# Kernel tuning notes

Measured on AMD Instinct MI355X. Metric: run time of the kernel, lower is better.

The kernel has to match this reference:

```python
import jax, jax.numpy as jnp
import numpy as np

MULTI_INFER_NUM = 8
D_EMBED = 128
T, B = 512, 32


def setup_inputs() -> dict:
    key = jax.random.key(0)
    k1, k2, k3 = jax.random.split(key, 3)
    positions = jax.random.randint(k1, (T, B), 0, 16, dtype=jnp.int64)
    outputs = jax.random.normal(k2, (T, B, D_EMBED), dtype=jnp.float32)
    table = jax.random.normal(k3, (MULTI_INFER_NUM + 1, D_EMBED, D_EMBED), dtype=jnp.float32)
    return {"positions": positions, "outputs": outputs, "table": table}


def reference(positions, outputs, table):
    # clip positions >= multi_infer_num to the sentinel row multi_infer_num
    r_positions = jnp.where(positions < MULTI_INFER_NUM, positions, MULTI_INFER_NUM)
    # gather per-(t,b) d x d transfer matrices: [T, B, d, d]
    positions_embedding = table[r_positions]
    # batched matvec: [T, B, d]
    transferred = jnp.einsum('ibde,ibd->ibe', positions_embedding, outputs)
    return transferred
```

## Files before the change

kernel.cpp:

```cpp
#include <hip/hip_runtime.h>
#include <hip/hip_bf16.h>

#define TBPAIRS 16384
#define DEMB    128
#define NR      9
#define CAP     16384
#define GRID2   512

#define BPACK_U4    (NR * 2048)
#define BPACK_BYTES (BPACK_U4 * 16)

#define LSTRIDE 130

using short8 = __attribute__((ext_vector_type(8))) short;
using f32x4  = __attribute__((ext_vector_type(4))) float;

__device__ __forceinline__ unsigned short f2bf(float f) {
    unsigned u = __float_as_uint(f);
    u = u + 0x7FFFu + ((u >> 16) & 1u);
    return (unsigned short)(u >> 16);
}

__global__ __launch_bounds__(256) void prep_kernel(
    const int*   __restrict__ positions,
    const float* __restrict__ table,
    uint4* __restrict__ bpack,
    int*   __restrict__ gcnt,
    int*   __restrict__ perm) {

    const int bid = blockIdx.x;
    const int tid = threadIdx.x;

    if (bid < 64) {
        __shared__ int lcnt[NR];
        __shared__ int lbase[NR];
        if (tid < NR) lcnt[tid] = 0;
        __syncthreads();
        const int pair = bid * 256 + tid;
        const int p = positions[pair];
        const int r = (p < 8) ? p : 8;
        const int rank = atomicAdd(&lcnt[r], 1);
        __syncthreads();
        if (tid < NR) lbase[tid] = atomicAdd(&gcnt[tid], lcnt[tid]);
        __syncthreads();
        perm[r * CAP + lbase[r] + rank] = pair;
    } else {
        __shared__ unsigned short sm[32 * LSTRIDE];
        const int pid = bid - 64;
        const int r   = pid >> 2;
        const int ks  = pid & 3;
        const float* M = table + (r * DEMB + ks * 32) * DEMB;

#pragma unroll
        for (int f4 = 0; f4 < 4; ++f4) {
            const int id   = f4 * 256 + tid;
            const int row  = id >> 5;
            const int col4 = id & 31;
            const float4 v = ((const float4*)(M + row * DEMB))[col4];
            unsigned short* dst = &sm[row * LSTRIDE + col4 * 4];
            dst[0] = f2bf(v.x); dst[1] = f2bf(v.y);
            dst[2] = f2bf(v.z); dst[3] = f2bf(v.w);
        }
        __syncthreads();

#pragma unroll
        for (int f = 0; f < 2; ++f) {
            const int fid  = f * 256 + tid;
            const int nt   = fid >> 6;
            const int lane = fid & 63;
            const int e    = nt * 16 + (lane & 15);
            const int ld0  = (lane >> 4) * 8;
            union { unsigned short us[8]; uint4 v; } u;
#pragma unroll
            for (int j = 0; j < 8; ++j)
                u.us[j] = sm[(ld0 + j) * LSTRIDE + e];
            bpack[r * 2048 + nt * 256 + ks * 64 + lane] = u.v;
        }
    }
}

__global__ __launch_bounds__(256) void transfer_kernel(
    const float* __restrict__ x,
    const uint4* __restrict__ bpack,
    const int*   __restrict__ gcnt,
    const int*   __restrict__ perm,
    float*       __restrict__ out) {

    __shared__ int cs[NR];
    __shared__ int tp[NR + 1];

    const int tid = threadIdx.x;
    if (tid < NR) cs[tid] = gcnt[tid];
    __syncthreads();
    if (tid == 0) {
        int acc = 0;
#pragma unroll
        for (int r = 0; r < NR; ++r) { tp[r] = acc; acc += (cs[r] + 15) >> 4; }
        tp[NR] = acc;
    }
    __syncthreads();

    const int wave  = tid >> 6;
    const int lane  = tid & 63;
    const int m16   = lane & 15;
    const int quad  = lane >> 4;
    const int total = tp[NR];

    for (int T = blockIdx.x * 4 + wave; T < total; T += GRID2 * 4) {
        int r = 0;
#pragma unroll
        for (int rr = 1; rr < NR; ++rr) r = (T >= tp[rr]) ? rr : r;
        const int tb = (T - tp[r]) * 16;
        const int c  = cs[r];
        const int nm = c - tb;
        const int* pr = perm + r * CAP + tb;

        const int slotA = pr[(m16 < nm) ? m16 : 0];
        const float* xrow = x + (size_t)slotA * DEMB;
        short8 a[4];
#pragma unroll
        for (int ks = 0; ks < 4; ++ks) {
            const float4* s4 = (const float4*)(xrow + ks * 32 + quad * 8);
            const float4 f0 = s4[0];
            const float4 f1 = s4[1];
            union { unsigned short us[8]; short8 s8; } ua;
            ua.us[0] = f2bf(f0.x); ua.us[1] = f2bf(f0.y);
            ua.us[2] = f2bf(f0.z); ua.us[3] = f2bf(f0.w);
            ua.us[4] = f2bf(f1.x); ua.us[5] = f2bf(f1.y);
            ua.us[6] = f2bf(f1.z); ua.us[7] = f2bf(f1.w);
            a[ks] = ua.s8;
        }

        int  prow[4];
        bool pval[4];
#pragma unroll
        for (int i = 0; i < 4; ++i) {
            const int m = quad * 4 + i;
            pval[i] = m < nm;
            prow[i] = pval[i] ? pr[m] : 0;
        }

        const uint4* bp = bpack + r * 2048 + lane;
#pragma unroll 2
        for (int nt = 0; nt < 8; ++nt) {
            f32x4 acc = {0.f, 0.f, 0.f, 0.f};
#pragma unroll
            for (int ks = 0; ks < 4; ++ks) {
                union { uint4 v4; short8 s8; } ub;
                ub.v4 = bp[(nt * 4 + ks) * 64];
                acc = __builtin_amdgcn_mfma_f32_16x16x32_bf16(a[ks], ub.s8, acc, 0, 0, 0);
            }
            const int col = nt * 16 + m16;
#pragma unroll
            for (int i = 0; i < 4; ++i)
                if (pval[i])
                    __builtin_nontemporal_store(acc[i], &out[(size_t)prow[i] * DEMB + col]);
        }
    }
}

extern "C" void kernel_launch(void* const* d_in, const int* in_sizes, int n_in,
                              void* d_out, int out_size, void* d_ws, size_t ws_size,
                              hipStream_t stream) {
    const int*   positions = (const int*)d_in[0];
    const float* outputs   = (const float*)d_in[1];
    const float* table     = (const float*)d_in[2];
    float* out = (float*)d_out;

    uint4* bpack = (uint4*)d_ws;
    int*   gcnt  = (int*)((char*)d_ws + BPACK_BYTES);
    int*   perm  = (int*)((char*)d_ws + BPACK_BYTES + 64);

    hipMemsetAsync((void*)gcnt, 0, 64, stream);
    hipLaunchKernelGGL(prep_kernel, dim3(100), dim3(256), 0, stream,
                       positions, table, bpack, gcnt, perm);
    hipLaunchKernelGGL(transfer_kernel, dim3(GRID2), dim3(256), 0, stream,
                       outputs, bpack, gcnt, perm, out);
}
```

Before: 75.84 us.

## Replace global atomic bucketing with per-block counts and prefix-sum lookup

Removes the global atomic counters and the memset launch. Each prep block now writes its row indices into its own fixed slot of the permutation buffer and stores per-block counts. The transfer kernel rebuilds prefix sums in shared memory and finds each pair by binary search. It also shares row indices across lanes with shuffles, and switches the output stores from nontemporal to normal stores. The cost is redundant prefix work in every transfer block, but one host-side launch and a serialization point go away.

```diff
diff --git a/kernel.cpp b/kernel.cpp
--- a/kernel.cpp
+++ b/kernel.cpp
@@ -1,5 +1,4 @@
 #include <hip/hip_runtime.h>
-#include <hip/hip_bf16.h>
 
 #define TBPAIRS 16384
 #define DEMB    128
@@ -9,6 +8,7 @@
 
 #define BPACK_U4    (NR * 2048)
 #define BPACK_BYTES (BPACK_U4 * 16)
+#define CNTS_BYTES  (64 * 16 * 4)
 
 #define LSTRIDE 130
 
@@ -25,7 +25,7 @@
     const int*   __restrict__ positions,
     const float* __restrict__ table,
     uint4* __restrict__ bpack,
-    int*   __restrict__ gcnt,
+    int*   __restrict__ cnts,
     int*   __restrict__ perm) {
 
     const int bid = blockIdx.x;
@@ -33,17 +33,15 @@
 
     if (bid < 64) {
         __shared__ int lcnt[NR];
-        __shared__ int lbase[NR];
         if (tid < NR) lcnt[tid] = 0;
         __syncthreads();
         const int pair = bid * 256 + tid;
         const int p = positions[pair];
         const int r = (p < 8) ? p : 8;
         const int rank = atomicAdd(&lcnt[r], 1);
+        perm[r * CAP + bid * 256 + rank] = pair;
         __syncthreads();
-        if (tid < NR) lbase[tid] = atomicAdd(&gcnt[tid], lcnt[tid]);
-        __syncthreads();
-        perm[r * CAP + lbase[r] + rank] = pair;
+        if (tid < NR) cnts[bid * 16 + tid] = lcnt[tid];
     } else {
         __shared__ unsigned short sm[32 * LSTRIDE];
         const int pid = bid - 64;
@@ -82,15 +80,27 @@
 __global__ __launch_bounds__(256) void transfer_kernel(
     const float* __restrict__ x,
     const uint4* __restrict__ bpack,
-    const int*   __restrict__ gcnt,
+    const int*   __restrict__ cnts,
     const int*   __restrict__ perm,
     float*       __restrict__ out) {
 
+    __shared__ int scnt[64 * 16];
+    __shared__ int pfx[NR][65];
     __shared__ int cs[NR];
     __shared__ int tp[NR + 1];
 
     const int tid = threadIdx.x;
-    if (tid < NR) cs[tid] = gcnt[tid];
+
+    ((int4*)scnt)[tid] = ((const int4*)cnts)[tid];
+    __syncthreads();
+
+    if (tid < NR) {
+        int acc = 0;
+#pragma unroll
+        for (int b = 0; b < 64; ++b) { pfx[tid][b] = acc; acc += scnt[b * 16 + tid]; }
+        pfx[tid][64] = acc;
+        cs[tid] = acc;
+    }
     __syncthreads();
     if (tid == 0) {
         int acc = 0;
@@ -111,11 +121,19 @@
 #pragma unroll
         for (int rr = 1; rr < NR; ++rr) r = (T >= tp[rr]) ? rr : r;
         const int tb = (T - tp[r]) * 16;
-        const int c  = cs[r];
-        const int nm = c - tb;
-        const int* pr = perm + r * CAP + tb;
+        const int nm = cs[r] - tb;
 
-        const int slotA = pr[(m16 < nm) ? m16 : 0];
+        const int g = tb + ((m16 < nm) ? m16 : 0);
+        int lo = 0, hi = 64;
+#pragma unroll
+        for (int it = 0; it < 6; ++it) {
+            const int mid = (lo + hi) >> 1;
+            const bool le = (pfx[r][mid] <= g);
+            lo = le ? mid : lo;
+            hi = le ? hi : mid;
+        }
+        const int slotA = perm[r * CAP + lo * 256 + (g - pfx[r][lo])];
+
         const float* xrow = x + (size_t)slotA * DEMB;
         short8 a[4];
 #pragma unroll
@@ -137,7 +155,7 @@
         for (int i = 0; i < 4; ++i) {
             const int m = quad * 4 + i;
             pval[i] = m < nm;
-            prow[i] = pval[i] ? pr[m] : 0;
+            prow[i] = __shfl(slotA, (lane & 48) | m, 64);
         }
 
         const uint4* bp = bpack + r * 2048 + lane;
@@ -154,7 +172,7 @@
 #pragma unroll
             for (int i = 0; i < 4; ++i)
                 if (pval[i])
-                    __builtin_nontemporal_store(acc[i], &out[(size_t)prow[i] * DEMB + col]);
+                    out[(size_t)prow[i] * DEMB + col] = acc[i];
         }
     }
 }
@@ -168,12 +186,11 @@
     float* out = (float*)d_out;
 
     uint4* bpack = (uint4*)d_ws;
-    int*   gcnt  = (int*)((char*)d_ws + BPACK_BYTES);
-    int*   perm  = (int*)((char*)d_ws + BPACK_BYTES + 64);
+    int*   cnts  = (int*)((char*)d_ws + BPACK_BYTES);
+    int*   perm  = (int*)((char*)d_ws + BPACK_BYTES + CNTS_BYTES);
 
-    hipMemsetAsync((void*)gcnt, 0, 64, stream);
     hipLaunchKernelGGL(prep_kernel, dim3(100), dim3(256), 0, stream,
-                       positions, table, bpack, gcnt, perm);
+                       positions, table, bpack, cnts, perm);
     hipLaunchKernelGGL(transfer_kernel, dim3(GRID2), dim3(256), 0, stream,
-                       outputs, bpack, gcnt, perm, out);
+                       outputs, bpack, cnts, perm, out);
 }
```

Result: no change. 76.06 us (+0.3%).
